# Performance work log

Hardware: AMD Instinct MI355X
Metric: run time of the kernel (lower is better)

Reference implementation:

```python
import jax, jax.numpy as jnp
import numpy as np
import math

HIDDEN = 2048
N_HEADS = 16
HEAD_DIM = HIDDEN // N_HEADS
ROPE_BASE = 10000.0


def setup_inputs() -> dict:
    key = jax.random.key(0)
    ks = jax.random.split(key, 5)
    B, S = 2, 2048
    hidden_states = jax.random.normal(ks[0], (B, S, HIDDEN), dtype=jnp.float32)
    # additive causal mask (bsz, 1, q_len, kv_len)
    causal = jnp.tril(jnp.ones((S, S), dtype=bool))
    attention_mask = jnp.where(causal, 0.0, jnp.finfo(jnp.float32).min)[None, None].astype(jnp.float32)
    attention_mask = jnp.broadcast_to(attention_mask, (B, 1, S, S))
    position_ids = jnp.broadcast_to(jnp.arange(S, dtype=jnp.int32)[None], (B, S))
    scale = 1.0 / math.sqrt(HIDDEN)
    Wq = jax.random.normal(ks[1], (HIDDEN, HIDDEN), dtype=jnp.float32) * scale
    Wk = jax.random.normal(ks[2], (HIDDEN, HIDDEN), dtype=jnp.float32) * scale
    Wv = jax.random.normal(ks[3], (HIDDEN, HIDDEN), dtype=jnp.float32) * scale
    Wo = jax.random.normal(ks[4], (HIDDEN, HIDDEN), dtype=jnp.float32) * scale
    return {"hidden_states": hidden_states, "attention_mask": attention_mask,
            "position_ids": position_ids, "Wq": Wq, "Wk": Wk, "Wv": Wv, "Wo": Wo}


def _rotate_half(x):
    x1, x2 = jnp.split(x, 2, axis=-1)
    return jnp.concatenate([-x2, x1], axis=-1)


def _rope_cos_sin(position_ids, head_dim, dtype):
    inv_freq = 1.0 / (ROPE_BASE ** (jnp.arange(0, head_dim, 2, dtype=jnp.float32) / head_dim))
    freqs = position_ids.astype(jnp.float32)[..., None] * inv_freq  # [B, S, hd/2]
    emb = jnp.concatenate([freqs, freqs], axis=-1)                  # [B, S, hd]
    # unsqueeze head dim -> [B, 1, S, hd]
    return jnp.cos(emb)[:, None].astype(dtype), jnp.sin(emb)[:, None].astype(dtype)


def reference(hidden_states, attention_mask, position_ids, Wq, Wk, Wv, Wo):
    B, S, _ = hidden_states.shape
    H, D = N_HEADS, HEAD_DIM
    # projections (nn.Linear: x @ W.T); split heads -> [B, H, S, D]
    def proj(W):
        return jnp.einsum('bsh,oh->bso', hidden_states, W).reshape(B, S, H, D).transpose(0, 2, 1, 3)
    q, k, v = proj(Wq), proj(Wk), proj(Wv)
    cos, sin = _rope_cos_sin(position_ids, D, hidden_states.dtype)
    q = q * cos + _rotate_half(q) * sin
    k = k * cos + _rotate_half(k) * sin
    scores = jnp.einsum('bhqd,bhkd->bhqk', q, k) / math.sqrt(D)
    scores = scores + attention_mask
    probs = jax.nn.softmax(scores.astype(jnp.float32), axis=-1).astype(q.dtype)
    attn = jnp.einsum('bhqk,bhkd->bhqd', probs, v)
    attn = attn.transpose(0, 2, 1, 3).reshape(B, S, H * D)
    return jnp.einsum('bso,ho->bsh', attn, Wo)
```

## Files before the change

### kernel.cpp

```cpp
#include <hip/hip_runtime.h>
#include <cstdint>

typedef unsigned short u16t;
typedef float v4f __attribute__((ext_vector_type(4)));
typedef short v8s __attribute__((ext_vector_type(8)));

#define HIDDEN 2048
#define NHEAD 16
#define HDIM 128
#define SEQ 2048
#define BATCH 2
#define MROWS (BATCH * SEQ)

__device__ __forceinline__ float bf2f(u16t u) {
  return __builtin_bit_cast(float, (uint32_t)((uint32_t)u << 16));
}
__device__ __forceinline__ u16t f2bf(float f) {
  uint32_t u = __builtin_bit_cast(uint32_t, f);
  u += 0x7FFFu + ((u >> 16) & 1u);
  return (u16t)(u >> 16);
}
__device__ __forceinline__ ushort4 f2bf4(float4 v) {
  ushort4 r;
  r.x = f2bf(v.x); r.y = f2bf(v.y); r.z = f2bf(v.z); r.w = f2bf(v.w);
  return r;
}

__device__ __forceinline__ void gld_lds16(const u16t* g, u16t* l) {
  __builtin_amdgcn_global_load_lds(
      (const __attribute__((address_space(1))) uint32_t*)g,
      (__attribute__((address_space(3))) uint32_t*)l, 16, 0, 0);
}

__global__ __launch_bounds__(256) void cvt_bf16(const float* __restrict__ src,
                                                u16t* __restrict__ dst, int n8) {
  int i = blockIdx.x * 256 + threadIdx.x;
  if (i < n8) {
    float4 a = ((const float4*)src)[2 * i];
    float4 b = ((const float4*)src)[2 * i + 1];
    union { ushort4 h[2]; uint4 u; } pk;
    pk.h[0] = f2bf4(a);
    pk.h[1] = f2bf4(b);
    ((uint4*)dst)[i] = pk.u;
  }
}

template <int B_BF16, int OUT_F32>
__global__ __launch_bounds__(256) void gemm_a16(const u16t* __restrict__ A,
                                                const void* __restrict__ Bp,
                                                void* __restrict__ Cp) {
  __shared__ u16t As[128 * 32];
  __shared__ u16t Bs[128 * 32];

  const int n0 = blockIdx.x * 128;
  const int m0 = blockIdx.y * 128;
  const int t = threadIdx.x;
  const int lane = t & 63;
  const int w = t >> 6;
  const int wm = w & 1;
  const int wn = w >> 1;
  const int l15 = lane & 15;
  const int quad = lane >> 4;

  v4f acc[4][4];
#pragma unroll
  for (int i = 0; i < 4; ++i)
#pragma unroll
    for (int j = 0; j < 4; ++j) acc[i][j] = (v4f){0.f, 0.f, 0.f, 0.f};

  for (int kb = 0; kb < HIDDEN; kb += 32) {
#pragma unroll
    for (int j = 0; j < 2; ++j) {
      int idx = t + j * 256;
      int row = idx >> 2;
      int ch = (idx & 3) * 8;
      gld_lds16(&A[(size_t)(m0 + row) * HIDDEN + kb + ch], &As[idx * 8]);
      if (B_BF16)
        gld_lds16(&((const u16t*)Bp)[(size_t)(n0 + row) * HIDDEN + kb + ch], &Bs[idx * 8]);
    }
    if (!B_BF16) {
      const float* B = (const float*)Bp;
#pragma unroll
      for (int j = 0; j < 4; ++j) {
        int idx = t + j * 256;
        int row = idx >> 3;
        int c4 = (idx & 7) * 4;
        float4 bv = *(const float4*)&B[(size_t)(n0 + row) * HIDDEN + kb + c4];
        *(ushort4*)&Bs[row * 32 + c4] = f2bf4(bv);
      }
    }
    __syncthreads();

    v8s af[4], bf[4];
#pragma unroll
    for (int mt = 0; mt < 4; ++mt)
      af[mt] = *(const v8s*)&As[(wm * 64 + mt * 16 + l15) * 32 + quad * 8];
#pragma unroll
    for (int nt = 0; nt < 4; ++nt)
      bf[nt] = *(const v8s*)&Bs[(wn * 64 + nt * 16 + l15) * 32 + quad * 8];

#pragma unroll
    for (int mt = 0; mt < 4; ++mt)
#pragma unroll
      for (int nt = 0; nt < 4; ++nt)
        acc[mt][nt] = __builtin_amdgcn_mfma_f32_16x16x32_bf16(af[mt], bf[nt], acc[mt][nt], 0, 0, 0);
    __syncthreads();
  }

#pragma unroll
  for (int mt = 0; mt < 4; ++mt) {
#pragma unroll
    for (int nt = 0; nt < 4; ++nt) {
      int col = n0 + wn * 64 + nt * 16 + l15;
#pragma unroll
      for (int r = 0; r < 4; ++r) {
        int row = m0 + wm * 64 + mt * 16 + quad * 4 + r;
        if (OUT_F32)
          ((float*)Cp)[(size_t)row * HIDDEN + col] = acc[mt][nt][r];
        else
          ((u16t*)Cp)[(size_t)row * HIDDEN + col] = f2bf(acc[mt][nt][r]);
      }
    }
  }
}

template <int B_BF16>
__global__ __launch_bounds__(256) void gemm_vt(const u16t* __restrict__ A,
                                               const void* __restrict__ Bp,
                                               u16t* __restrict__ VtOut) {
  __shared__ u16t As[128 * 32];
  __shared__ u16t Bs[128 * 32];
  __shared__ u16t Ct[128 * 136];

  const int n0 = blockIdx.x * 128;
  const int m0 = blockIdx.y * 128;
  const int t = threadIdx.x;
  const int lane = t & 63;
  const int w = t >> 6;
  const int wm = w & 1;
  const int wn = w >> 1;
  const int l15 = lane & 15;
  const int quad = lane >> 4;

  v4f acc[4][4];
#pragma unroll
  for (int i = 0; i < 4; ++i)
#pragma unroll
    for (int j = 0; j < 4; ++j) acc[i][j] = (v4f){0.f, 0.f, 0.f, 0.f};

  for (int kb = 0; kb < HIDDEN; kb += 32) {
#pragma unroll
    for (int j = 0; j < 2; ++j) {
      int idx = t + j * 256;
      int row = idx >> 2;
      int ch = (idx & 3) * 8;
      gld_lds16(&A[(size_t)(m0 + row) * HIDDEN + kb + ch], &As[idx * 8]);
      if (B_BF16)
        gld_lds16(&((const u16t*)Bp)[(size_t)(n0 + row) * HIDDEN + kb + ch], &Bs[idx * 8]);
    }
    if (!B_BF16) {
      const float* B = (const float*)Bp;
#pragma unroll
      for (int j = 0; j < 4; ++j) {
        int idx = t + j * 256;
        int row = idx >> 3;
        int c4 = (idx & 7) * 4;
        float4 bv = *(const float4*)&B[(size_t)(n0 + row) * HIDDEN + kb + c4];
        *(ushort4*)&Bs[row * 32 + c4] = f2bf4(bv);
      }
    }
    __syncthreads();

    v8s af[4], bf[4];
#pragma unroll
    for (int mt = 0; mt < 4; ++mt)
      af[mt] = *(const v8s*)&As[(wm * 64 + mt * 16 + l15) * 32 + quad * 8];
#pragma unroll
    for (int nt = 0; nt < 4; ++nt)
      bf[nt] = *(const v8s*)&Bs[(wn * 64 + nt * 16 + l15) * 32 + quad * 8];

#pragma unroll
    for (int mt = 0; mt < 4; ++mt)
#pragma unroll
      for (int nt = 0; nt < 4; ++nt)
        acc[mt][nt] = __builtin_amdgcn_mfma_f32_16x16x32_bf16(af[mt], bf[nt], acc[mt][nt], 0, 0, 0);
    __syncthreads();
  }

#pragma unroll
  for (int mt = 0; mt < 4; ++mt)
#pragma unroll
    for (int nt = 0; nt < 4; ++nt)
#pragma unroll
      for (int r = 0; r < 4; ++r)
        Ct[(wn * 64 + nt * 16 + l15) * 136 + (wm * 64 + mt * 16 + quad * 4 + r)] =
            f2bf(acc[mt][nt][r]);
  __syncthreads();

#pragma unroll
  for (int j = 0; j < 8; ++j) {
    int idx = t + j * 256;
    int nl = idx >> 4;
    int mc = idx & 15;
    *(uint4*)&VtOut[(size_t)(n0 + nl) * MROWS + m0 + mc * 8] =
        *(const uint4*)&Ct[nl * 136 + mc * 8];
  }
}

__global__ __launch_bounds__(256) void rope_k(u16t* __restrict__ q, u16t* __restrict__ k) {
  int idx = blockIdx.x * 256 + threadIdx.x;
  int i = idx & 63;
  int h = (idx >> 6) & (NHEAD - 1);
  int m = idx >> 10;
  int s = m & (SEQ - 1);
  float inv = __expf(-(float)i * 0.14391156831212787f);
  float th = (float)s * inv;
  float sn, cs;
  __sincosf(th, &sn, &cs);
  size_t base = (size_t)m * HIDDEN + h * HDIM + i;
  {
    float a = bf2f(q[base]), b = bf2f(q[base + 64]);
    q[base] = f2bf(a * cs - b * sn);
    q[base + 64] = f2bf(b * cs + a * sn);
  }
  {
    float a = bf2f(k[base]), b = bf2f(k[base + 64]);
    k[base] = f2bf(a * cs - b * sn);
    k[base + 64] = f2bf(b * cs + a * sn);
  }
}

__global__ __launch_bounds__(512) void flash2(const u16t* __restrict__ Q,
                                              const u16t* __restrict__ K,
                                              const u16t* __restrict__ Vt,
                                              u16t* __restrict__ O) {
  __shared__ u16t smem[27136];
  u16t* Ks = smem;
  u16t* Vs = smem + 8704;
  u16t* Ps = smem + 17920;

  const int a = blockIdx.x;
  const int bh = blockIdx.y;
  const int b = bh >> 4;
  const int h = bh & 15;
  const size_t rowb = (size_t)b * SEQ;
  const u16t* vtg = Vt + (size_t)h * HDIM * MROWS + (size_t)b * SEQ;

  const int t = threadIdx.x;
  const int lane = t & 63;
  const int w = t >> 6;
  const int l15 = lane & 15;
  const int quad = lane >> 4;
  const float C2 = 0.12751743f;
  const float NEG = -3.0e38f;

  for (int half = 0; half < 2; ++half) {
    const int qt = half ? (15 - a) : a;
    const int q0 = qt * 128;

#pragma unroll
    for (int j = 0; j < 4; ++j) {
      int idx = t + j * 512;
      int row = idx >> 4;
      int ch = (idx & 15) * 8;
      *(uint4*)&smem[row * 136 + ch] =
          *(const uint4*)&Q[(rowb + q0 + row) * HIDDEN + h * HDIM + ch];
    }
    __syncthreads();
    v8s qf[4];
#pragma unroll
    for (int ks = 0; ks < 4; ++ks)
      qf[ks] = *(const v8s*)&smem[(w * 16 + l15) * 136 + ks * 32 + quad * 8];
    __syncthreads();

    float mi[4], li[4];
    v4f o[8];
#pragma unroll
    for (int r = 0; r < 4; ++r) { mi[r] = NEG; li[r] = 0.f; }
#pragma unroll
    for (int nt = 0; nt < 8; ++nt) o[nt] = (v4f){0.f, 0.f, 0.f, 0.f};

    const int nsteps = 2 * (qt + 1);
    for (int kt = 0; kt < nsteps; ++kt) {
      const int kv0 = kt * 64;
#pragma unroll
      for (int j = 0; j < 2; ++j) {
        int idx = t + j * 512;
        int kr = idx >> 4;
        int ch = (idx & 15) * 8;
        *(uint4*)&Ks[kr * 136 + ch] =
            *(const uint4*)&K[(rowb + kv0 + kr) * HIDDEN + h * HDIM + ch];
        int d = idx >> 3;
        int kc = (idx & 7) * 8;
        *(uint4*)&Vs[d * 72 + kc] = *(const uint4*)&vtg[(size_t)d * MROWS + kv0 + kc];
      }
      __syncthreads();

      v4f sc[4];
#pragma unroll
      for (int nt = 0; nt < 4; ++nt) {
        sc[nt] = (v4f){0.f, 0.f, 0.f, 0.f};
#pragma unroll
        for (int ks = 0; ks < 4; ++ks) {
          v8s kf = *(const v8s*)&Ks[(nt * 16 + l15) * 136 + ks * 32 + quad * 8];
          sc[nt] = __builtin_amdgcn_mfma_f32_16x16x32_bf16(qf[ks], kf, sc[nt], 0, 0, 0);
        }
      }

      const bool mm = (kv0 + 64 > q0);
#pragma unroll
      for (int r = 0; r < 4; ++r) {
        int row_g = q0 + w * 16 + quad * 4 + r;
        float sv[4];
#pragma unroll
        for (int nt = 0; nt < 4; ++nt) {
          sv[nt] = sc[nt][r];
          if (mm && (kv0 + nt * 16 + l15 > row_g)) sv[nt] = NEG;
        }
        float rm = fmaxf(fmaxf(sv[0], sv[1]), fmaxf(sv[2], sv[3]));
#pragma unroll
        for (int off = 1; off < 16; off <<= 1) rm = fmaxf(rm, __shfl_xor(rm, off));
        float mn = fmaxf(mi[r], rm);
        float alpha = exp2f((mi[r] - mn) * C2);
        float ps = 0.f;
        u16t pb[4];
#pragma unroll
        for (int nt = 0; nt < 4; ++nt) {
          float p = exp2f((sv[nt] - mn) * C2);
          ps += p;
          pb[nt] = f2bf(p);
        }
#pragma unroll
        for (int off = 1; off < 16; off <<= 1) ps += __shfl_xor(ps, off);
        li[r] = li[r] * alpha + ps;
        mi[r] = mn;
#pragma unroll
        for (int nt = 0; nt < 8; ++nt) o[nt][r] *= alpha;
        int pr = (w * 16 + quad * 4 + r) * 72;
#pragma unroll
        for (int nt = 0; nt < 4; ++nt) Ps[pr + nt * 16 + l15] = pb[nt];
      }

#pragma unroll
      for (int ks = 0; ks < 2; ++ks) {
        v8s pf = *(const v8s*)&Ps[(w * 16 + l15) * 72 + ks * 32 + quad * 8];
#pragma unroll
        for (int nt = 0; nt < 8; ++nt) {
          v8s vf = *(const v8s*)&Vs[(nt * 16 + l15) * 72 + ks * 32 + quad * 8];
          o[nt] = __builtin_amdgcn_mfma_f32_16x16x32_bf16(pf, vf, o[nt], 0, 0, 0);
        }
      }
      __syncthreads();
    }

#pragma unroll
    for (int r = 0; r < 4; ++r) {
      float inv = 1.0f / li[r];
      size_t row = rowb + q0 + w * 16 + quad * 4 + r;
#pragma unroll
      for (int nt = 0; nt < 8; ++nt)
        O[row * HIDDEN + h * HDIM + nt * 16 + l15] = f2bf(o[nt][r] * inv);
    }
    __syncthreads();
  }
}

extern "C" void kernel_launch(void* const* d_in, const int* in_sizes, int n_in,
                              void* d_out, int out_size, void* d_ws, size_t ws_size,
                              hipStream_t stream) {
  const float* X = (const float*)d_in[0];
  const float* Wq = (const float*)d_in[3];
  const float* Wk = (const float*)d_in[4];
  const float* Wv = (const float*)d_in[5];
  const float* Wo = (const float*)d_in[6];
  float* out = (float*)d_out;

  char* wsb = (char*)d_ws;
  const size_t MB = 1024 * 1024;
  u16t* xb = (u16t*)(wsb + 0 * MB);
  u16t* q = (u16t*)(wsb + 16 * MB);
  u16t* k = (u16t*)(wsb + 32 * MB);
  u16t* vt = (u16t*)(wsb + 48 * MB);
  u16t* a = xb;

  dim3 blk(256);
  dim3 gg(HIDDEN / 128, MROWS / 128);
  dim3 fg(8, BATCH * NHEAD);
  const int XN8 = MROWS * HIDDEN / 8;
  const int WN8 = HIDDEN * HIDDEN / 8;

  cvt_bf16<<<(XN8 + 255) / 256, blk, 0, stream>>>(X, xb, XN8);

  if (ws_size >= 96 * MB) {
    u16t* wqb = (u16t*)(wsb + 64 * MB);
    u16t* wkb = (u16t*)(wsb + 72 * MB);
    u16t* wvb = (u16t*)(wsb + 80 * MB);
    u16t* wob = (u16t*)(wsb + 88 * MB);
    cvt_bf16<<<(WN8 + 255) / 256, blk, 0, stream>>>(Wq, wqb, WN8);
    cvt_bf16<<<(WN8 + 255) / 256, blk, 0, stream>>>(Wk, wkb, WN8);
    cvt_bf16<<<(WN8 + 255) / 256, blk, 0, stream>>>(Wv, wvb, WN8);
    cvt_bf16<<<(WN8 + 255) / 256, blk, 0, stream>>>(Wo, wob, WN8);

    gemm_a16<1, 0><<<gg, blk, 0, stream>>>(xb, wqb, q);
    gemm_a16<1, 0><<<gg, blk, 0, stream>>>(xb, wkb, k);
    gemm_vt<1><<<gg, blk, 0, stream>>>(xb, wvb, vt);
    rope_k<<<(MROWS * NHEAD * 64) / 256, blk, 0, stream>>>(q, k);
    flash2<<<fg, dim3(512), 0, stream>>>(q, k, vt, a);
    gemm_a16<1, 1><<<gg, blk, 0, stream>>>(a, wob, out);
  } else {
    gemm_a16<0, 0><<<gg, blk, 0, stream>>>(xb, Wq, q);
    gemm_a16<0, 0><<<gg, blk, 0, stream>>>(xb, Wk, k);
    gemm_vt<0><<<gg, blk, 0, stream>>>(xb, Wv, vt);
    rope_k<<<(MROWS * NHEAD * 64) / 256, blk, 0, stream>>>(q, k);
    flash2<<<fg, dim3(512), 0, stream>>>(q, k, vt, a);
    gemm_a16<0, 1><<<gg, blk, 0, stream>>>(a, Wo, out);
  }
}
```

Baseline: 515.7 us.

## Double-buffer flash attention K/V tiles with register prefetch and XOR swizzle

The flash attention kernel now keeps two LDS buffers for the K/V tiles and prefetches the next tile into registers while the current one is computed. This removes one barrier per iteration and hides global load latency. Padded LDS strides are replaced with XOR-swizzled layouts for K, V and P, and the causal mask check is hoisted out of the inner loop. The four weight-conversion launches are merged into one kernel. LDS use grows to 80 KB per block, which may reduce occupancy.

```diff
diff --git a/kernel.cpp b/kernel.cpp
--- a/kernel.cpp
+++ b/kernel.cpp
@@ -43,6 +43,24 @@
     pk.h[1] = f2bf4(b);
     ((uint4*)dst)[i] = pk.u;
   }
+}
+
+__global__ __launch_bounds__(256) void cvt_bf16_w4(
+    const float* __restrict__ s0, const float* __restrict__ s1,
+    const float* __restrict__ s2, const float* __restrict__ s3,
+    u16t* __restrict__ d0, u16t* __restrict__ d1,
+    u16t* __restrict__ d2, u16t* __restrict__ d3) {
+  int i = blockIdx.x * 256 + threadIdx.x;
+  int sel = i >> 19;
+  int j = i & 0x7FFFF;
+  const float* src = (sel == 0) ? s0 : (sel == 1) ? s1 : (sel == 2) ? s2 : s3;
+  u16t* dst = (sel == 0) ? d0 : (sel == 1) ? d1 : (sel == 2) ? d2 : d3;
+  float4 a = ((const float4*)src)[2 * j];
+  float4 b = ((const float4*)src)[2 * j + 1];
+  union { ushort4 h[2]; uint4 u; } pk;
+  pk.h[0] = f2bf4(a);
+  pk.h[1] = f2bf4(b);
+  ((uint4*)dst)[j] = pk.u;
 }
 
 template <int B_BF16, int OUT_F32>
@@ -234,10 +252,8 @@
                                               const u16t* __restrict__ K,
                                               const u16t* __restrict__ Vt,
                                               u16t* __restrict__ O) {
-  __shared__ u16t smem[27136];
-  u16t* Ks = smem;
-  u16t* Vs = smem + 8704;
-  u16t* Ps = smem + 17920;
+  __shared__ u16t smem[40960];
+  u16t* Ps = smem + 32768;
 
   const int a = blockIdx.x;
   const int bh = blockIdx.y;
@@ -251,12 +267,28 @@
   const int w = t >> 6;
   const int l15 = lane & 15;
   const int quad = lane >> 4;
+  const int l7 = l15 & 7;
   const float C2 = 0.12751743f;
   const float NEG = -3.0e38f;
+
+  const int krow = t >> 4;
+  const int kch = (t & 15) * 8;
+  const int vrow = t >> 3;
+  const int vch = (t & 7) * 8;
+  const int kx = kch ^ ((krow & 7) * 8);
+  const int vx = vch ^ ((vrow & 7) * 8);
+  const u16t* Kgb = &K[(rowb + krow) * HIDDEN + h * HDIM + kch];
+  const u16t* Vgb = vtg + (size_t)vrow * MROWS + vch;
 
   for (int half = 0; half < 2; ++half) {
     const int qt = half ? (15 - a) : a;
     const int q0 = qt * 128;
+    const int nsteps = 2 * (qt + 1);
+
+    uint4 ck0 = *(const uint4*)Kgb;
+    uint4 ck1 = *(const uint4*)(Kgb + 32 * HIDDEN);
+    uint4 cv0 = *(const uint4*)Vgb;
+    uint4 cv1 = *(const uint4*)(Vgb + (size_t)64 * MROWS);
 
 #pragma unroll
     for (int j = 0; j < 4; ++j) {
@@ -280,29 +312,33 @@
 #pragma unroll
     for (int nt = 0; nt < 8; ++nt) o[nt] = (v4f){0.f, 0.f, 0.f, 0.f};
 
-    const int nsteps = 2 * (qt + 1);
     for (int kt = 0; kt < nsteps; ++kt) {
+      u16t* Kb = smem + (kt & 1) * 16384;
+      u16t* Vb = Kb + 8192;
+      *(uint4*)&Kb[krow * 128 + kx] = ck0;
+      *(uint4*)&Kb[(krow + 32) * 128 + kx] = ck1;
+      *(uint4*)&Vb[vrow * 64 + vx] = cv0;
+      *(uint4*)&Vb[(vrow + 64) * 64 + vx] = cv1;
+      if (kt + 1 < nsteps) {
+        const int kv1 = (kt + 1) * 64;
+        const u16t* kg = Kgb + (size_t)kv1 * HIDDEN;
+        ck0 = *(const uint4*)kg;
+        ck1 = *(const uint4*)(kg + 32 * HIDDEN);
+        const u16t* vg = Vgb + kv1;
+        cv0 = *(const uint4*)vg;
+        cv1 = *(const uint4*)(vg + (size_t)64 * MROWS);
+      }
+      __syncthreads();
+
       const int kv0 = kt * 64;
-#pragma unroll
-      for (int j = 0; j < 2; ++j) {
-        int idx = t + j * 512;
-        int kr = idx >> 4;
-        int ch = (idx & 15) * 8;
-        *(uint4*)&Ks[kr * 136 + ch] =
-            *(const uint4*)&K[(rowb + kv0 + kr) * HIDDEN + h * HDIM + ch];
-        int d = idx >> 3;
-        int kc = (idx & 7) * 8;
-        *(uint4*)&Vs[d * 72 + kc] = *(const uint4*)&vtg[(size_t)d * MROWS + kv0 + kc];
-      }
-      __syncthreads();
-
       v4f sc[4];
 #pragma unroll
       for (int nt = 0; nt < 4; ++nt) {
         sc[nt] = (v4f){0.f, 0.f, 0.f, 0.f};
 #pragma unroll
         for (int ks = 0; ks < 4; ++ks) {
-          v8s kf = *(const v8s*)&Ks[(nt * 16 + l15) * 136 + ks * 32 + quad * 8];
+          v8s kf = *(const v8s*)&Kb[(nt * 16 + l15) * 128 +
+                                    ((ks * 32 + quad * 8) ^ (l7 * 8))];
           sc[nt] = __builtin_amdgcn_mfma_f32_16x16x32_bf16(qf[ks], kf, sc[nt], 0, 0, 0);
         }
       }
@@ -310,12 +346,14 @@
       const bool mm = (kv0 + 64 > q0);
 #pragma unroll
       for (int r = 0; r < 4; ++r) {
-        int row_g = q0 + w * 16 + quad * 4 + r;
         float sv[4];
 #pragma unroll
-        for (int nt = 0; nt < 4; ++nt) {
-          sv[nt] = sc[nt][r];
-          if (mm && (kv0 + nt * 16 + l15 > row_g)) sv[nt] = NEG;
+        for (int nt = 0; nt < 4; ++nt) sv[nt] = sc[nt][r];
+        if (mm) {
+          int row_g = q0 + w * 16 + quad * 4 + r;
+#pragma unroll
+          for (int nt = 0; nt < 4; ++nt)
+            if (kv0 + nt * 16 + l15 > row_g) sv[nt] = NEG;
         }
         float rm = fmaxf(fmaxf(sv[0], sv[1]), fmaxf(sv[2], sv[3]));
 #pragma unroll
@@ -336,21 +374,24 @@
         mi[r] = mn;
 #pragma unroll
         for (int nt = 0; nt < 8; ++nt) o[nt][r] *= alpha;
-        int pr = (w * 16 + quad * 4 + r) * 72;
-#pragma unroll
-        for (int nt = 0; nt < 4; ++nt) Ps[pr + nt * 16 + l15] = pb[nt];
+        int rowp = w * 16 + quad * 4 + r;
+        int psw = (rowp & 7) * 8;
+#pragma unroll
+        for (int nt = 0; nt < 4; ++nt)
+          Ps[rowp * 64 + ((nt * 16 + l15) ^ psw)] = pb[nt];
       }
 
 #pragma unroll
       for (int ks = 0; ks < 2; ++ks) {
-        v8s pf = *(const v8s*)&Ps[(w * 16 + l15) * 72 + ks * 32 + quad * 8];
+        v8s pf = *(const v8s*)&Ps[(w * 16 + l15) * 64 +
+                                  ((ks * 32 + quad * 8) ^ (l7 * 8))];
 #pragma unroll
         for (int nt = 0; nt < 8; ++nt) {
-          v8s vf = *(const v8s*)&Vs[(nt * 16 + l15) * 72 + ks * 32 + quad * 8];
+          v8s vf = *(const v8s*)&Vb[(nt * 16 + l15) * 64 +
+                                    ((ks * 32 + quad * 8) ^ (l7 * 8))];
           o[nt] = __builtin_amdgcn_mfma_f32_16x16x32_bf16(pf, vf, o[nt], 0, 0, 0);
         }
       }
-      __syncthreads();
     }
 
 #pragma unroll
@@ -396,10 +437,7 @@
     u16t* wkb = (u16t*)(wsb + 72 * MB);
     u16t* wvb = (u16t*)(wsb + 80 * MB);
     u16t* wob = (u16t*)(wsb + 88 * MB);
-    cvt_bf16<<<(WN8 + 255) / 256, blk, 0, stream>>>(Wq, wqb, WN8);
-    cvt_bf16<<<(WN8 + 255) / 256, blk, 0, stream>>>(Wk, wkb, WN8);
-    cvt_bf16<<<(WN8 + 255) / 256, blk, 0, stream>>>(Wv, wvb, WN8);
-    cvt_bf16<<<(WN8 + 255) / 256, blk, 0, stream>>>(Wo, wob, WN8);
+    cvt_bf16_w4<<<(4 * WN8) / 256, blk, 0, stream>>>(Wq, Wk, Wv, Wo, wqb, wkb, wvb, wob);
 
     gemm_a16<1, 0><<<gg, blk, 0, stream>>>(xb, wqb, q);
     gemm_a16<1, 0><<<gg, blk, 0, stream>>>(xb, wkb, k);
```

After: 456.0 us. -11.6%, faster.
